# Optimization experiments

Measured on AMD Instinct MI355X. Metric: run time of the kernel, lower is better.

Reference implementation:

```python
import jax, jax.numpy as jnp
import numpy as np

NVOC = 32000
DIM = 512
HID = 512
NLAYERS = 2
SEQ = 128
BATCH = 32


def setup_inputs() -> dict:
    key = jax.random.key(0)
    ks = jax.random.split(key, 8)
    tokens = jax.random.randint(ks[0], (SEQ, BATCH), 0, NVOC, dtype=jnp.int32)
    emb = jax.random.uniform(ks[1], (NVOC, DIM), minval=-0.1, maxval=0.1, dtype=jnp.float32)
    # xavier-uniform-ish init for gate matrices
    def xav(k, shape):
        fan_in, fan_out = shape[1], shape[0]
        lim = jnp.sqrt(6.0 / (fan_in + fan_out))
        return jax.random.uniform(k, shape, minval=-lim, maxval=lim, dtype=jnp.float32)
    W0 = xav(ks[2], (4 * HID, DIM))     # layer 0 input weights
    W1 = xav(ks[3], (4 * HID, HID))     # layer 1 input weights
    U0 = xav(ks[4], (4 * HID, HID))
    U1 = xav(ks[5], (4 * HID, HID))
    b = jnp.zeros((4 * HID,), jnp.float32)
    dec_w = jax.random.uniform(ks[6], (NVOC, HID), minval=-0.1, maxval=0.1, dtype=jnp.float32)
    dec_b = jnp.zeros((NVOC,), jnp.float32)
    return {"tokens": tokens, "emb": emb, "W0": W0, "W1": W1,
            "U0": U0, "U1": U1, "b": b, "dec_w": dec_w, "dec_b": dec_b}


def _lstm_forward(tokens, emb, W0, W1, U0, U1, b, dec_w, dec_b):
    # dropout in eval mode (identity)
    x = emb[tokens]  # [S, B, DIM]
    Ws = [W0, W1]
    Us = [U0, U1]
    h0 = jnp.zeros((NLAYERS, BATCH, HID), x.dtype)
    c0 = jnp.zeros((NLAYERS, BATCH, HID), x.dtype)

    def step(carry, x_t):
        h_tot, c_tot = carry
        new_h, new_c = [], []
        inp = x_t
        for l in range(NLAYERS):
            gates = inp @ Ws[l].T + h_tot[l] @ Us[l].T + b  # [B, 4H]
            i_g, f_g, g_g, o_g = jnp.split(gates, 4, axis=1)
            i_g = jax.nn.sigmoid(i_g)
            f_g = jax.nn.sigmoid(f_g)
            o_g = jax.nn.sigmoid(o_g)
            g_g = jnp.tanh(g_g)
            c_new = f_g * c_tot[l] + i_g * g_g
            h_new = o_g * jnp.tanh(c_new)
            new_h.append(h_new)
            new_c.append(c_new)
            inp = h_new
        return (jnp.stack(new_h), jnp.stack(new_c)), new_h[-1]

    (_, _), outs = jax.lax.scan(step, (h0, c0), x)  # outs: [S, B, HID]
    decoded = outs @ dec_w.T + dec_b  # [S, B, NVOC]
    return decoded


def reference(tokens, emb, W0, W1, U0, U1, b, dec_w, dec_b):
    return _lstm_forward(tokens, emb, W0, W1, U0, U1, b, dec_w, dec_b)
```

## Files before the change

### kernel.cpp

```cpp
#include <hip/hip_runtime.h>
#include <hip/hip_bf16.h>


#define NVOC 32000
#define DIM  512
#define HID  512
#define SEQ  128
#define BAT  32
#define NB   64
#define NDEC 192
#define NTILE (32 * 250)
#define SLOT (BAT * HID)

typedef short s8v __attribute__((ext_vector_type(8)));
typedef short s4v __attribute__((ext_vector_type(4)));
typedef float f4v __attribute__((ext_vector_type(4)));
typedef unsigned long long u64;

__device__ __forceinline__ short f2bf(float f) {
    unsigned u = __builtin_bit_cast(unsigned, f);
    unsigned r = (u + 0x7fffu + ((u >> 16) & 1u)) >> 16;
    return (short)r;
}
__device__ __forceinline__ float bf2f(short s) {
    unsigned u = ((unsigned)(unsigned short)s) << 16;
    return __builtin_bit_cast(float, u);
}
__device__ __forceinline__ float sigm(float x) { return 1.f / (1.f + __expf(-x)); }
__device__ __forceinline__ float ftanh(float x) {
    float e = __expf(2.f * x);
    return 1.f - 2.f / (e + 1.f);
}

__device__ __forceinline__ f4v mf16(s8v a, s8v b, f4v c) {
    return __builtin_amdgcn_mfma_f32_16x16x32_bf16(a, b, c, 0, 0, 0);
}

__device__ __forceinline__ u64 cohload8(const short* p) {
    return __hip_atomic_load((const u64*)p, __ATOMIC_RELAXED,
                             __HIP_MEMORY_SCOPE_AGENT);
}
__device__ __forceinline__ void cohstore2(short* p, unsigned short v) {
    __hip_atomic_store((unsigned short*)p, v, __ATOMIC_RELAXED,
                       __HIP_MEMORY_SCOPE_AGENT);
}

__device__ __forceinline__ bool hasSent(u64 v) {
    u64 n = ~v;
    return ((n - 0x0001000100010001ull) & ~n & 0x8000800080008000ull) != 0ull;
}

__device__ __forceinline__ void poll32s(const unsigned* f, int l, unsigned tgt) {
    const unsigned* p = f + (l & 31);
    while (true) {
        unsigned v = __hip_atomic_load(p, __ATOMIC_RELAXED,
                                       __HIP_MEMORY_SCOPE_AGENT);
        if (__all((int)(v >= tgt))) break;
        __builtin_amdgcn_s_sleep(16);
    }
}

__global__ __launch_bounds__(256) void prep_dec(const float* __restrict__ dw,
                                                short* __restrict__ dbf)
{
    int id = blockIdx.x * 256 + threadIdx.x;
    if (id >= (NVOC * DIM) / 4) return;
    int e = id * 4;
    float4 v = *(const float4*)(dw + e);
    s4v o; o[0] = f2bf(v.x); o[1] = f2bf(v.y); o[2] = f2bf(v.z); o[3] = f2bf(v.w);
    *(s4v*)(dbf + e) = o;
}

__global__ __launch_bounds__(256) void prep_w0(const float* __restrict__ W0,
                                               short* __restrict__ w0h,
                                               short* __restrict__ w0l)
{
    int id = blockIdx.x * 256 + threadIdx.x;
    if (id >= 2048 * 512) return;
    float v = W0[id];
    short h = f2bf(v);
    w0h[id] = h;
    w0l[id] = f2bf(v - bf2f(h));
}

__global__ __launch_bounds__(256) void embed_k(const int* __restrict__ toks,
                                               const float* __restrict__ emb,
                                               short* __restrict__ xemb)
{
    int id = blockIdx.x * 256 + threadIdx.x;
    if (id >= (SEQ * BAT * DIM) / 4) return;
    int e  = id * 4;
    int tb = e >> 9;
    int k4 = e & 511;
    int tok = toks[tb];
    float4 v = *(const float4*)(emb + (size_t)tok * DIM + k4);
    s4v o; o[0] = f2bf(v.x); o[1] = f2bf(v.y); o[2] = f2bf(v.z); o[3] = f2bf(v.w);
    *(s4v*)(xemb + e) = o;
}

__global__ __launch_bounds__(256) void init_k(short* __restrict__ hbuf,
                                              unsigned* __restrict__ bar)
{
    int id = blockIdx.x * 256 + threadIdx.x;
    const int ringU64 = 129 * SLOT / 4;
    if (id < 2 * ringU64) {
        int r = id % ringU64;
        u64 v = (r < SLOT / 4) ? 0ull : 0xFFFFFFFFFFFFFFFFull;
        ((u64*)hbuf)[id] = v;
    }
    if (id < 64) bar[id] = 0;
}

__global__ __launch_bounds__(256) void gx_gemm(
    const short* __restrict__ A,
    const short* __restrict__ Bh,
    const short* __restrict__ Bl,
    float* __restrict__ out)
{
    const int nb = blockIdx.x & 15, mb = blockIdx.x >> 4;
    const int m0 = mb * 128, n0 = nb * 128;
    __shared__ short Alds[128][40];
    __shared__ short Bhl[128][40];
    __shared__ short Bll[128][40];
    const int tid = threadIdx.x, l = tid & 63, w = tid >> 6;
    const int wr = w >> 1, wc = w & 1;
    const int lr = l & 15, kg = l >> 4;

    f4v acc[4][4];
    #pragma unroll
    for (int mi = 0; mi < 4; ++mi)
        #pragma unroll
        for (int ni = 0; ni < 4; ++ni) {
            acc[mi][ni][0] = 0.f; acc[mi][ni][1] = 0.f;
            acc[mi][ni][2] = 0.f; acc[mi][ni][3] = 0.f;
        }

    for (int kt = 0; kt < 16; ++kt) {
        #pragma unroll
        for (int i = 0; i < 2; ++i) {
            int c = tid + i * 256;
            int row = c >> 2, q = (c & 3) << 3;
            *(s8v*)&Alds[row][q] = *(const s8v*)(A  + (size_t)(m0 + row) * 512 + kt * 32 + q);
            *(s8v*)&Bhl[row][q]  = *(const s8v*)(Bh + (size_t)(n0 + row) * 512 + kt * 32 + q);
            *(s8v*)&Bll[row][q]  = *(const s8v*)(Bl + (size_t)(n0 + row) * 512 + kt * 32 + q);
        }
        __syncthreads();
        s8v af[4], bhf[4], blf[4];
        #pragma unroll
        for (int i = 0; i < 4; ++i) {
            af[i]  = *(const s8v*)&Alds[wr * 64 + i * 16 + lr][kg * 8];
            bhf[i] = *(const s8v*)&Bhl[wc * 64 + i * 16 + lr][kg * 8];
            blf[i] = *(const s8v*)&Bll[wc * 64 + i * 16 + lr][kg * 8];
        }
        #pragma unroll
        for (int mi = 0; mi < 4; ++mi)
            #pragma unroll
            for (int ni = 0; ni < 4; ++ni) {
                acc[mi][ni] = mf16(af[mi], bhf[ni], acc[mi][ni]);
                acc[mi][ni] = mf16(af[mi], blf[ni], acc[mi][ni]);
            }
        __syncthreads();
    }

    #pragma unroll
    for (int mi = 0; mi < 4; ++mi)
        #pragma unroll
        for (int ni = 0; ni < 4; ++ni) {
            int n = n0 + wc * 64 + ni * 16 + lr;
            #pragma unroll
            for (int r = 0; r < 4; ++r) {
                int m = m0 + wr * 64 + mi * 16 + kg * 4 + r;
                out[(size_t)m * 2048 + n] = acc[mi][ni][r];
            }
        }
}

__global__ __launch_bounds__(512, 1) void rnn_k(
    const float* __restrict__ W1f, const float* __restrict__ U0f,
    const float* __restrict__ U1f,
    const float* __restrict__ bias,
    const float* __restrict__ Gx,
    short* __restrict__ hbuf,
    short* __restrict__ adec,
    const short* __restrict__ dbf,
    const float* __restrict__ db,
    float* __restrict__ out,
    unsigned* __restrict__ bar)
{
    const int tid = threadIdx.x;
    const int bx  = blockIdx.x;
    const int w2  = tid >> 6;
    const int l   = tid & 63;
    const int lr  = l & 15;
    const int kg  = l >> 4;

    __shared__ short Alds[32][520];
    __shared__ float gbuf[2][4][16][33];
    __shared__ float pbuf[2][4][16][33];
    __shared__ s8v AdT[4][132];
    __shared__ s8v BdT[4][132];

    if (bx >= NB) {
        const int d  = bx - NB;
        const int wm = w2 >> 2;
        const int wn = w2 & 3;
        const int drow = tid >> 2, dq = tid & 3;
        int lastmb = -1;
        for (int tile = d; tile < NTILE; tile += NDEC) {
            const int mb = tile / 250, nbt = tile - mb * 250;
            const int m0 = mb * 128, n0 = nbt * 128;
            if (mb != lastmb) {
                if (w2 == 0) poll32s(bar + 32, l, (unsigned)(4 * mb + 5));
                __syncthreads();
                lastmb = mb;
            }
            f4v acc[4][2];
            #pragma unroll
            for (int mi = 0; mi < 4; ++mi)
                #pragma unroll
                for (int ni = 0; ni < 2; ++ni) {
                    acc[mi][ni][0] = 0.f; acc[mi][ni][1] = 0.f;
                    acc[mi][ni][2] = 0.f; acc[mi][ni][3] = 0.f;
                }
            for (int kt = 0; kt < 16; ++kt) {
                AdT[dq][drow] = *(const s8v*)(adec + (size_t)(m0 + drow) * 512 + kt * 32 + dq * 8);
                BdT[dq][drow] = *(const s8v*)(dbf  + (size_t)(n0 + drow) * 512 + kt * 32 + dq * 8);
                __syncthreads();
                s8v af[4], bfr[2];
                #pragma unroll
                for (int i = 0; i < 4; ++i)
                    af[i] = AdT[kg][wm * 64 + i * 16 + lr];
                #pragma unroll
                for (int j = 0; j < 2; ++j)
                    bfr[j] = BdT[kg][wn * 32 + j * 16 + lr];
                #pragma unroll
                for (int mi = 0; mi < 4; ++mi)
                    #pragma unroll
                    for (int ni = 0; ni < 2; ++ni)
                        acc[mi][ni] = mf16(af[mi], bfr[ni], acc[mi][ni]);
                __syncthreads();
            }
            #pragma unroll
            for (int mi = 0; mi < 4; ++mi)
                #pragma unroll
                for (int ni = 0; ni < 2; ++ni) {
                    int n = n0 + wn * 32 + ni * 16 + lr;
                    float bb = db[n];
                    #pragma unroll
                    for (int r = 0; r < 4; ++r) {
                        int m = m0 + wm * 64 + mi * 16 + kg * 4 + r;
                        out[(size_t)m * NVOC + n] = acc[mi][ni][r] + bb;
                    }
                }
        }
        return;
    }

    const int bl    = bx;
    const int layer = bl >> 5;
    const int j0    = (bl & 31) * 16;
    const int g     = w2 & 3;
    const int kh    = w2 >> 2;

    const int eb = tid >> 4;
    const int ej = tid & 15;
    const int jj = j0 + ej;
    const float bi = bias[jj];
    const float bf_ = bias[512 + jj];
    const float bg = bias[1024 + jj];
    const float bo = bias[1536 + jj];
    float cst = 0.f;

    short* ring0 = hbuf;
    short* ring1 = hbuf + 129 * SLOT;

    auto stageS = [&](const short* s) {
        u64 va[8];
        #pragma unroll
        for (int i = 0; i < 8; ++i) {
            int c = tid + i * 512;
            va[i] = cohload8(s + (c >> 7) * HID + (c & 127) * 4);
        }
        #pragma unroll
        for (int i = 0; i < 8; ++i) {
            int c = tid + i * 512;
            while (hasSent(va[i]))
                va[i] = cohload8(s + (c >> 7) * HID + (c & 127) * 4);
            *(u64*)&Alds[c >> 7][(c & 127) * 4] = va[i];
        }
    };
    auto mfma8 = [&](const s8v* WH, const s8v* WL, float (&dst)[2][4][16][33]) {
        f4v a0h = {0.f, 0.f, 0.f, 0.f};
        f4v a0l = a0h, a1h = a0h, a1l = a0h;
        #pragma unroll
        for (int ks = 0; ks < 8; ++ks) {
            const int k = kh * 256 + ks * 32 + kg * 8;
            s8v a0 = *(const s8v*)&Alds[lr][k];
            s8v a1 = *(const s8v*)&Alds[16 + lr][k];
            a0h = mf16(a0, WH[ks], a0h);
            a0l = mf16(a0, WL[ks], a0l);
            a1h = mf16(a1, WH[ks], a1h);
            a1l = mf16(a1, WL[ks], a1l);
        }
        #pragma unroll
        for (int r = 0; r < 4; ++r) {
            dst[kh][g][lr][kg * 4 + r]      = a0h[r] + a0l[r];
            dst[kh][g][lr][16 + kg * 4 + r] = a1h[r] + a1l[r];
        }
    };
    const int gr = g * 512 + j0 + lr;
    auto loadw = [&](const float* M, s8v* WH, s8v* WL) {
        #pragma unroll
        for (int ks = 0; ks < 8; ++ks) {
            const float* src = M + (size_t)gr * 512 + kh * 256 + ks * 32 + kg * 8;
            float4 va = *(const float4*)src;
            float4 vb = *(const float4*)(src + 4);
            float vv[8] = {va.x, va.y, va.z, va.w, vb.x, vb.y, vb.z, vb.w};
            s8v hi, lo;
            #pragma unroll
            for (int e = 0; e < 8; ++e) {
                short h = f2bf(vv[e]);
                hi[e] = h; lo[e] = f2bf(vv[e] - bf2f(h));
            }
            WH[ks] = hi; WL[ks] = lo;
        }
    };

    if (layer == 0) {
        s8v wh[8], wl[8];
        loadw(U0f, wh, wl);
        for (int it = 0; it < SEQ; ++it) {
            const float* gp = Gx + ((size_t)it * BAT + eb) * 2048 + jj;
            float gx0 = gp[0], gx1 = gp[512], gx2 = gp[1024], gx3 = gp[1536];
            stageS(ring0 + (size_t)it * SLOT);
            __syncthreads();
            mfma8(wh, wl, gbuf);
            __syncthreads();
            float si = gbuf[0][0][ej][eb] + gbuf[1][0][ej][eb] + gx0;
            float sf = gbuf[0][1][ej][eb] + gbuf[1][1][ej][eb] + gx1;
            float sg = gbuf[0][2][ej][eb] + gbuf[1][2][ej][eb] + gx2;
            float so = gbuf[0][3][ej][eb] + gbuf[1][3][ej][eb] + gx3;
            float gi = sigm(si + bi);
            float gf = sigm(sf + bf_);
            float gg = ftanh(sg + bg);
            float go = sigm(so + bo);
            cst = gf * cst + gi * gg;
            unsigned short hs = (unsigned short)f2bf(go * ftanh(cst));
            cohstore2(ring0 + (size_t)(it + 1) * SLOT + eb * HID + jj, hs);
        }
    } else {
        s8v whU[8], wlU[8], whW[8], wlW[8];
        loadw(U1f, whU, wlU);
        loadw(W1f, whW, wlW);
        stageS(ring0 + 1 * SLOT);
        __syncthreads();
        mfma8(whW, wlW, pbuf);
        for (int it = 1; it <= SEQ; ++it) {
            stageS(ring1 + (size_t)(it - 1) * SLOT);
            __syncthreads();
            mfma8(whU, wlU, gbuf);
            __syncthreads();
            float si = gbuf[0][0][ej][eb] + gbuf[1][0][ej][eb]
                     + pbuf[0][0][ej][eb] + pbuf[1][0][ej][eb];
            float sf = gbuf[0][1][ej][eb] + gbuf[1][1][ej][eb]
                     + pbuf[0][1][ej][eb] + pbuf[1][1][ej][eb];
            float sg = gbuf[0][2][ej][eb] + gbuf[1][2][ej][eb]
                     + pbuf[0][2][ej][eb] + pbuf[1][2][ej][eb];
            float so = gbuf[0][3][ej][eb] + gbuf[1][3][ej][eb]
                     + pbuf[0][3][ej][eb] + pbuf[1][3][ej][eb];
            float gi = sigm(si + bi);
            float gf = sigm(sf + bf_);
            float gg = ftanh(sg + bg);
            float go = sigm(so + bo);
            cst = gf * cst + gi * gg;
            unsigned short hs = (unsigned short)f2bf(go * ftanh(cst));
            cohstore2(ring1 + (size_t)it * SLOT + eb * HID + jj, hs);
            cohstore2(adec + ((size_t)(it - 1) * BAT + eb) * HID + jj, hs);
            if ((it & 3) == 0 || it == SEQ) {
                asm volatile("s_waitcnt vmcnt(0)" ::: "memory");
                __syncthreads();
                if (tid == 0)
                    __hip_atomic_store(bar + 32 + (bl & 31), (unsigned)(it + 1),
                                       __ATOMIC_RELAXED, __HIP_MEMORY_SCOPE_AGENT);
            }
            if (it < SEQ) {
                stageS(ring0 + (size_t)(it + 1) * SLOT);
                __syncthreads();
                mfma8(whW, wlW, pbuf);
            }
        }
    }
}

extern "C" void kernel_launch(void* const* d_in, const int* in_sizes, int n_in,
                              void* d_out, int out_size, void* d_ws, size_t ws_size,
                              hipStream_t stream)
{
    const int*   toks = (const int*)d_in[0];
    const float* emb  = (const float*)d_in[1];
    const float* W0   = (const float*)d_in[2];
    const float* W1   = (const float*)d_in[3];
    const float* U0   = (const float*)d_in[4];
    const float* U1   = (const float*)d_in[5];
    const float* bias = (const float*)d_in[6];
    const float* dw   = (const float*)d_in[7];
    const float* db   = (const float*)d_in[8];
    float* out = (float*)d_out;

    char* ws = (char*)d_ws;
    size_t off = 0;
    auto alloc = [&](size_t bytes) -> void* {
        void* p = ws + off;
        off += (bytes + 255) & ~(size_t)255;
        return p;
    };
    short*    dbf  = (short*)alloc((size_t)NVOC * DIM * 2);
    short*    xemb = (short*)alloc((size_t)SEQ * BAT * DIM * 2);
    short*    w0h  = (short*)alloc(2048ull * 512 * 2);
    short*    w0l  = (short*)alloc(2048ull * 512 * 2);
    float*    Gx   = (float*)alloc((size_t)SEQ * BAT * 2048 * 4);
    short*    hbuf = (short*)alloc(2ull * 129 * SLOT * 2);
    short*    adec = (short*)alloc((size_t)SEQ * BAT * HID * 2);
    unsigned* bar  = (unsigned*)alloc(256);

    prep_dec<<<(NVOC * DIM / 4 + 255) / 256, 256, 0, stream>>>(dw, dbf);
    prep_w0 <<<(2048 * 512 + 255) / 256, 256, 0, stream>>>(W0, w0h, w0l);
    embed_k <<<(SEQ * BAT * DIM / 4 + 255) / 256, 256, 0, stream>>>(toks, emb, xemb);
    {
        int ringU64 = 2 * 129 * SLOT / 4;
        init_k<<<(ringU64 + 255) / 256, 256, 0, stream>>>(hbuf, bar);
    }

    gx_gemm<<<32 * 16, 256, 0, stream>>>(xemb, w0h, w0l, Gx);

    rnn_k<<<NB + NDEC, 512, 0, stream>>>(W1, U0, U1, bias, Gx, hbuf, adec,
                                         dbf, db, out, bar);
}
```

Baseline: 699.0 us.

## Merge layer-1 input and recurrent staging into one phase with double-buffered projections

Layer 1 now issues the loads for both its own previous h and layer 0's next h together, stages them side by side in a widened LDS tile, and runs both MFMA passes between a single pair of barriers. The input projection results are double-buffered by parity, so the next step's projection is computed in the same phase as the current recurrence. This removes one stage/sync/MFMA round per timestep from the serial critical path. Row ownership and the per-thread (batch, hidden) mapping are also remapped so each wave owns four units across all four gates, and in layer 0 the Gx loads are placed between issuing and committing the h loads. The cost is more LDS per block and a longer per-step MFMA phase.

```diff
diff --git a/kernel.cpp b/kernel.cpp
--- a/kernel.cpp
+++ b/kernel.cpp
@@ -194,9 +194,9 @@
     const int lr  = l & 15;
     const int kg  = l >> 4;
 
-    __shared__ short Alds[32][520];
-    __shared__ float gbuf[2][4][16][33];
-    __shared__ float pbuf[2][4][16][33];
+    __shared__ short Alds[32][1032];
+    __shared__ float S[2][4][16][33];
+    __shared__ float P[2][2][4][16][33];
     __shared__ s8v AdT[4][132];
     __shared__ s8v BdT[4][132];
 
@@ -259,12 +259,12 @@
     const int bl    = bx;
     const int layer = bl >> 5;
     const int j0    = (bl & 31) * 16;
-    const int g     = w2 & 3;
+    const int wq    = w2 & 3;
     const int kh    = w2 >> 2;
 
-    const int eb = tid >> 4;
-    const int ej = tid & 15;
-    const int jj = j0 + ej;
+    const int jq = l >> 4;
+    const int b  = (l & 15) + kh * 16;
+    const int jj = j0 + wq * 4 + jq;
     const float bi = bias[jj];
     const float bf_ = bias[512 + jj];
     const float bg = bias[1024 + jj];
@@ -274,45 +274,27 @@
     short* ring0 = hbuf;
     short* ring1 = hbuf + 129 * SLOT;
 
-    auto stageS = [&](const short* s) {
-        u64 va[8];
+    auto issue8 = [&](const short* s, u64* va) {
         #pragma unroll
         for (int i = 0; i < 8; ++i) {
             int c = tid + i * 512;
             va[i] = cohload8(s + (c >> 7) * HID + (c & 127) * 4);
         }
+    };
+    auto commit8 = [&](const short* s, u64* va, int c0) {
         #pragma unroll
         for (int i = 0; i < 8; ++i) {
             int c = tid + i * 512;
             while (hasSent(va[i]))
                 va[i] = cohload8(s + (c >> 7) * HID + (c & 127) * 4);
-            *(u64*)&Alds[c >> 7][(c & 127) * 4] = va[i];
+            *(u64*)&Alds[c >> 7][c0 + (c & 127) * 4] = va[i];
         }
     };
-    auto mfma8 = [&](const s8v* WH, const s8v* WL, float (&dst)[2][4][16][33]) {
-        f4v a0h = {0.f, 0.f, 0.f, 0.f};
-        f4v a0l = a0h, a1h = a0h, a1l = a0h;
+    const int grow = (lr >> 2) * 512 + j0 + wq * 4 + (lr & 3);
+    auto loadw = [&](const float* M, s8v* WH, s8v* WL) {
         #pragma unroll
         for (int ks = 0; ks < 8; ++ks) {
-            const int k = kh * 256 + ks * 32 + kg * 8;
-            s8v a0 = *(const s8v*)&Alds[lr][k];
-            s8v a1 = *(const s8v*)&Alds[16 + lr][k];
-            a0h = mf16(a0, WH[ks], a0h);
-            a0l = mf16(a0, WL[ks], a0l);
-            a1h = mf16(a1, WH[ks], a1h);
-            a1l = mf16(a1, WL[ks], a1l);
-        }
-        #pragma unroll
-        for (int r = 0; r < 4; ++r) {
-            dst[kh][g][lr][kg * 4 + r]      = a0h[r] + a0l[r];
-            dst[kh][g][lr][16 + kg * 4 + r] = a1h[r] + a1l[r];
-        }
-    };
-    const int gr = g * 512 + j0 + lr;
-    auto loadw = [&](const float* M, s8v* WH, s8v* WL) {
-        #pragma unroll
-        for (int ks = 0; ks < 8; ++ks) {
-            const float* src = M + (size_t)gr * 512 + kh * 256 + ks * 32 + kg * 8;
+            const float* src = M + (size_t)grow * 512 + kh * 256 + ks * 32 + kg * 8;
             float4 va = *(const float4*)src;
             float4 vb = *(const float4*)(src + 4);
             float vv[8] = {va.x, va.y, va.z, va.w, vb.x, vb.y, vb.z, vb.w};
@@ -325,68 +307,98 @@
             WH[ks] = hi; WL[ks] = lo;
         }
     };
+    auto mfmaS = [&](const s8v* WH, const s8v* WL, int c0,
+                     float (&dst)[2][4][16][33]) {
+        f4v a0h = {0.f, 0.f, 0.f, 0.f};
+        f4v a0l = a0h, a1h = a0h, a1l = a0h;
+        #pragma unroll
+        for (int ks = 0; ks < 8; ++ks) {
+            const int k = c0 + ks * 32 + kg * 8;
+            s8v a0 = *(const s8v*)&Alds[lr][k];
+            s8v a1 = *(const s8v*)&Alds[16 + lr][k];
+            a0h = mf16(a0, WH[ks], a0h);
+            a0l = mf16(a0, WL[ks], a0l);
+            a1h = mf16(a1, WH[ks], a1h);
+            a1l = mf16(a1, WL[ks], a1l);
+        }
+        #pragma unroll
+        for (int r = 0; r < 4; ++r) {
+            dst[kh][wq][lr][kg * 4 + r]      = a0h[r] + a0l[r];
+            dst[kh][wq][lr][16 + kg * 4 + r] = a1h[r] + a1l[r];
+        }
+    };
 
     if (layer == 0) {
         s8v wh[8], wl[8];
         loadw(U0f, wh, wl);
         for (int it = 0; it < SEQ; ++it) {
-            const float* gp = Gx + ((size_t)it * BAT + eb) * 2048 + jj;
+            u64 va[8];
+            issue8(ring0 + (size_t)it * SLOT, va);
+            const float* gp = Gx + ((size_t)it * BAT + b) * 2048 + jj;
             float gx0 = gp[0], gx1 = gp[512], gx2 = gp[1024], gx3 = gp[1536];
-            stageS(ring0 + (size_t)it * SLOT);
-            __syncthreads();
-            mfma8(wh, wl, gbuf);
-            __syncthreads();
-            float si = gbuf[0][0][ej][eb] + gbuf[1][0][ej][eb] + gx0;
-            float sf = gbuf[0][1][ej][eb] + gbuf[1][1][ej][eb] + gx1;
-            float sg = gbuf[0][2][ej][eb] + gbuf[1][2][ej][eb] + gx2;
-            float so = gbuf[0][3][ej][eb] + gbuf[1][3][ej][eb] + gx3;
-            float gi = sigm(si + bi);
-            float gf = sigm(sf + bf_);
-            float gg = ftanh(sg + bg);
-            float go = sigm(so + bo);
+            commit8(ring0 + (size_t)it * SLOT, va, 0);
+            __syncthreads();
+            mfmaS(wh, wl, kh * 256, S);
+            __syncthreads();
+            float gvi = S[0][wq][0 * 4 + jq][b] + S[1][wq][0 * 4 + jq][b] + gx0;
+            float gvf = S[0][wq][1 * 4 + jq][b] + S[1][wq][1 * 4 + jq][b] + gx1;
+            float gvg = S[0][wq][2 * 4 + jq][b] + S[1][wq][2 * 4 + jq][b] + gx2;
+            float gvo = S[0][wq][3 * 4 + jq][b] + S[1][wq][3 * 4 + jq][b] + gx3;
+            float gi = sigm(gvi + bi);
+            float gf = sigm(gvf + bf_);
+            float gg = ftanh(gvg + bg);
+            float go = sigm(gvo + bo);
             cst = gf * cst + gi * gg;
             unsigned short hs = (unsigned short)f2bf(go * ftanh(cst));
-            cohstore2(ring0 + (size_t)(it + 1) * SLOT + eb * HID + jj, hs);
+            cohstore2(ring0 + (size_t)(it + 1) * SLOT + b * HID + jj, hs);
         }
     } else {
         s8v whU[8], wlU[8], whW[8], wlW[8];
         loadw(U1f, whU, wlU);
         loadw(W1f, whW, wlW);
-        stageS(ring0 + 1 * SLOT);
-        __syncthreads();
-        mfma8(whW, wlW, pbuf);
+        {
+            u64 va[8];
+            issue8(ring0 + 1 * SLOT, va);
+            commit8(ring0 + 1 * SLOT, va, 520);
+            __syncthreads();
+            mfmaS(whW, wlW, 520 + kh * 256, P[1]);
+            __syncthreads();
+        }
         for (int it = 1; it <= SEQ; ++it) {
-            stageS(ring1 + (size_t)(it - 1) * SLOT);
-            __syncthreads();
-            mfma8(whU, wlU, gbuf);
-            __syncthreads();
-            float si = gbuf[0][0][ej][eb] + gbuf[1][0][ej][eb]
-                     + pbuf[0][0][ej][eb] + pbuf[1][0][ej][eb];
-            float sf = gbuf[0][1][ej][eb] + gbuf[1][1][ej][eb]
-                     + pbuf[0][1][ej][eb] + pbuf[1][1][ej][eb];
-            float sg = gbuf[0][2][ej][eb] + gbuf[1][2][ej][eb]
-                     + pbuf[0][2][ej][eb] + pbuf[1][2][ej][eb];
-            float so = gbuf[0][3][ej][eb] + gbuf[1][3][ej][eb]
-                     + pbuf[0][3][ej][eb] + pbuf[1][3][ej][eb];
-            float gi = sigm(si + bi);
-            float gf = sigm(sf + bf_);
-            float gg = ftanh(sg + bg);
-            float go = sigm(so + bo);
+            const bool doH0 = (it < SEQ);
+            u64 vh1[8], vh0[8];
+            issue8(ring1 + (size_t)(it - 1) * SLOT, vh1);
+            if (doH0) issue8(ring0 + (size_t)(it + 1) * SLOT, vh0);
+            commit8(ring1 + (size_t)(it - 1) * SLOT, vh1, 0);
+            if (doH0) commit8(ring0 + (size_t)(it + 1) * SLOT, vh0, 520);
+            __syncthreads();
+            mfmaS(whU, wlU, kh * 256, S);
+            if (doH0) mfmaS(whW, wlW, 520 + kh * 256,
+                            P[(it + 1) & 1]);
+            __syncthreads();
+            const int par = it & 1;
+            float gvi = S[0][wq][0 * 4 + jq][b] + S[1][wq][0 * 4 + jq][b]
+                      + P[par][0][wq][0 * 4 + jq][b] + P[par][1][wq][0 * 4 + jq][b];
+            float gvf = S[0][wq][1 * 4 + jq][b] + S[1][wq][1 * 4 + jq][b]
+                      + P[par][0][wq][1 * 4 + jq][b] + P[par][1][wq][1 * 4 + jq][b];
+            float gvg = S[0][wq][2 * 4 + jq][b] + S[1][wq][2 * 4 + jq][b]
+                      + P[par][0][wq][2 * 4 + jq][b] + P[par][1][wq][2 * 4 + jq][b];
+            float gvo = S[0][wq][3 * 4 + jq][b] + S[1][wq][3 * 4 + jq][b]
+                      + P[par][0][wq][3 * 4 + jq][b] + P[par][1][wq][3 * 4 + jq][b];
+            float gi = sigm(gvi + bi);
+            float gf = sigm(gvf + bf_);
+            float gg = ftanh(gvg + bg);
+            float go = sigm(gvo + bo);
             cst = gf * cst + gi * gg;
             unsigned short hs = (unsigned short)f2bf(go * ftanh(cst));
-            cohstore2(ring1 + (size_t)it * SLOT + eb * HID + jj, hs);
-            cohstore2(adec + ((size_t)(it - 1) * BAT + eb) * HID + jj, hs);
+            cohstore2(ring1 + (size_t)it * SLOT + b * HID + jj, hs);
+            cohstore2(adec + ((size_t)(it - 1) * BAT + b) * HID + jj, hs);
             if ((it & 3) == 0 || it == SEQ) {
                 asm volatile("s_waitcnt vmcnt(0)" ::: "memory");
                 __syncthreads();
                 if (tid == 0)
                     __hip_atomic_store(bar + 32 + (bl & 31), (unsigned)(it + 1),
                                        __ATOMIC_RELAXED, __HIP_MEMORY_SCOPE_AGENT);
-            }
-            if (it < SEQ) {
-                stageS(ring0 + (size_t)(it + 1) * SLOT);
-                __syncthreads();
-                mfma8(whW, wlW, pbuf);
             }
         }
     }
```

Result: slower. 1.041 ms (+48.9%).

## Merge prep kernels into one launch and pack LSTM epilogue to two units per thread

Applied to the files above, without the earlier changes.

Combines the four preprocessing kernels (decoder weight cast, W0 hi/lo split, embedding gather, ring init) into a single launch dispatched by block index, removing three kernel launch gaps. In the recurrent kernel, the gate epilogue now runs on half the threads, each handling two adjacent hidden units with float2 Gx loads and one 32-bit packed coherent store instead of two 16-bit stores. Extra __syncthreads are added in layer 1 after the pbuf MFMA so the epilogue threads cannot race with the next pbuf write. This trades fewer, wider stores against idle threads in the epilogue and extra barriers on the serial critical path.

```diff
diff --git a/kernel.cpp b/kernel.cpp
--- a/kernel.cpp
+++ b/kernel.cpp
@@ -40,8 +40,8 @@
     return __hip_atomic_load((const u64*)p, __ATOMIC_RELAXED,
                              __HIP_MEMORY_SCOPE_AGENT);
 }
-__device__ __forceinline__ void cohstore2(short* p, unsigned short v) {
-    __hip_atomic_store((unsigned short*)p, v, __ATOMIC_RELAXED,
+__device__ __forceinline__ void cohstore4(short* p, unsigned v) {
+    __hip_atomic_store((unsigned*)p, v, __ATOMIC_RELAXED,
                        __HIP_MEMORY_SCOPE_AGENT);
 }
 
@@ -60,55 +60,46 @@
     }
 }
 
-__global__ __launch_bounds__(256) void prep_dec(const float* __restrict__ dw,
-                                                short* __restrict__ dbf)
+__global__ __launch_bounds__(256) void prep_all(
+    const float* __restrict__ dw, short* __restrict__ dbf,
+    const float* __restrict__ W0, short* __restrict__ w0h,
+    short* __restrict__ w0l,
+    const int* __restrict__ toks, const float* __restrict__ emb,
+    short* __restrict__ xemb,
+    short* __restrict__ hbuf, unsigned* __restrict__ bar)
 {
-    int id = blockIdx.x * 256 + threadIdx.x;
-    if (id >= (NVOC * DIM) / 4) return;
-    int e = id * 4;
-    float4 v = *(const float4*)(dw + e);
-    s4v o; o[0] = f2bf(v.x); o[1] = f2bf(v.y); o[2] = f2bf(v.z); o[3] = f2bf(v.w);
-    *(s4v*)(dbf + e) = o;
-}
-
-__global__ __launch_bounds__(256) void prep_w0(const float* __restrict__ W0,
-                                               short* __restrict__ w0h,
-                                               short* __restrict__ w0l)
-{
-    int id = blockIdx.x * 256 + threadIdx.x;
-    if (id >= 2048 * 512) return;
-    float v = W0[id];
-    short h = f2bf(v);
-    w0h[id] = h;
-    w0l[id] = f2bf(v - bf2f(h));
-}
-
-__global__ __launch_bounds__(256) void embed_k(const int* __restrict__ toks,
-                                               const float* __restrict__ emb,
-                                               short* __restrict__ xemb)
-{
-    int id = blockIdx.x * 256 + threadIdx.x;
-    if (id >= (SEQ * BAT * DIM) / 4) return;
-    int e  = id * 4;
-    int tb = e >> 9;
-    int k4 = e & 511;
-    int tok = toks[tb];
-    float4 v = *(const float4*)(emb + (size_t)tok * DIM + k4);
-    s4v o; o[0] = f2bf(v.x); o[1] = f2bf(v.y); o[2] = f2bf(v.z); o[3] = f2bf(v.w);
-    *(s4v*)(xemb + e) = o;
-}
-
-__global__ __launch_bounds__(256) void init_k(short* __restrict__ hbuf,
-                                              unsigned* __restrict__ bar)
-{
-    int id = blockIdx.x * 256 + threadIdx.x;
-    const int ringU64 = 129 * SLOT / 4;
-    if (id < 2 * ringU64) {
-        int r = id % ringU64;
-        u64 v = (r < SLOT / 4) ? 0ull : 0xFFFFFFFFFFFFFFFFull;
-        ((u64*)hbuf)[id] = v;
-    }
-    if (id < 64) bar[id] = 0;
+    const int b = blockIdx.x, tid = threadIdx.x;
+    if (b < 16000) {
+        int id = b * 256 + tid;
+        int e = id * 4;
+        float4 v = *(const float4*)(dw + e);
+        s4v o; o[0] = f2bf(v.x); o[1] = f2bf(v.y); o[2] = f2bf(v.z); o[3] = f2bf(v.w);
+        *(s4v*)(dbf + e) = o;
+    } else if (b < 20096) {
+        int id = (b - 16000) * 256 + tid;
+        float v = W0[id];
+        short h = f2bf(v);
+        w0h[id] = h;
+        w0l[id] = f2bf(v - bf2f(h));
+    } else if (b < 22144) {
+        int id = (b - 20096) * 256 + tid;
+        int e  = id * 4;
+        int tb = e >> 9;
+        int k4 = e & 511;
+        int tok = toks[tb];
+        float4 v = *(const float4*)(emb + (size_t)tok * DIM + k4);
+        s4v o; o[0] = f2bf(v.x); o[1] = f2bf(v.y); o[2] = f2bf(v.z); o[3] = f2bf(v.w);
+        *(s4v*)(xemb + e) = o;
+    } else {
+        int id = (b - 22144) * 256 + tid;
+        const int ringU64 = 129 * SLOT / 4;
+        if (id < 2 * ringU64) {
+            int r = id % ringU64;
+            u64 v = (r < SLOT / 4) ? 0ull : 0xFFFFFFFFFFFFFFFFull;
+            ((u64*)hbuf)[id] = v;
+        }
+        if (id < 64) bar[id] = 0;
+    }
 }
 
 __global__ __launch_bounds__(256) void gx_gemm(
@@ -259,17 +250,19 @@
     const int bl    = bx;
     const int layer = bl >> 5;
     const int j0    = (bl & 31) * 16;
-    const int g     = w2 & 3;
-    const int kh    = w2 >> 2;
-
-    const int eb = tid >> 4;
-    const int ej = tid & 15;
-    const int jj = j0 + ej;
-    const float bi = bias[jj];
-    const float bf_ = bias[512 + jj];
-    const float bg = bias[1024 + jj];
-    const float bo = bias[1536 + jj];
-    float cst = 0.f;
+
+    const bool epi = (tid < 256);
+    const int eb  = (tid >> 3) & 31;
+    const int ej  = (tid & 7) * 2;
+    const int jg0 = j0 + ej;
+    float bi0 = 0, bi1 = 0, bff0 = 0, bff1 = 0, bg0 = 0, bg1 = 0, bo0 = 0, bo1 = 0;
+    if (epi) {
+        bi0 = bias[jg0];         bi1 = bias[jg0 + 1];
+        bff0 = bias[512 + jg0];  bff1 = bias[512 + jg0 + 1];
+        bg0 = bias[1024 + jg0];  bg1 = bias[1024 + jg0 + 1];
+        bo0 = bias[1536 + jg0];  bo1 = bias[1536 + jg0 + 1];
+    }
+    float c0 = 0.f, c1 = 0.f;
 
     short* ring0 = hbuf;
     short* ring1 = hbuf + 129 * SLOT;
@@ -289,6 +282,8 @@
             *(u64*)&Alds[c >> 7][(c & 127) * 4] = va[i];
         }
     };
+    const int g  = w2 & 3;
+    const int kh = w2 >> 2;
     auto mfma8 = [&](const s8v* WH, const s8v* WL, float (&dst)[2][4][16][33]) {
         f4v a0h = {0.f, 0.f, 0.f, 0.f};
         f4v a0l = a0h, a1h = a0h, a1l = a0h;
@@ -330,23 +325,37 @@
         s8v wh[8], wl[8];
         loadw(U0f, wh, wl);
         for (int it = 0; it < SEQ; ++it) {
-            const float* gp = Gx + ((size_t)it * BAT + eb) * 2048 + jj;
-            float gx0 = gp[0], gx1 = gp[512], gx2 = gp[1024], gx3 = gp[1536];
+            float2 gxv0 = {0, 0}, gxv1 = {0, 0}, gxv2 = {0, 0}, gxv3 = {0, 0};
+            if (epi) {
+                const float* gp = Gx + ((size_t)it * BAT + eb) * 2048 + jg0;
+                gxv0 = *(const float2*)(gp);
+                gxv1 = *(const float2*)(gp + 512);
+                gxv2 = *(const float2*)(gp + 1024);
+                gxv3 = *(const float2*)(gp + 1536);
+            }
             stageS(ring0 + (size_t)it * SLOT);
             __syncthreads();
             mfma8(wh, wl, gbuf);
             __syncthreads();
-            float si = gbuf[0][0][ej][eb] + gbuf[1][0][ej][eb] + gx0;
-            float sf = gbuf[0][1][ej][eb] + gbuf[1][1][ej][eb] + gx1;
-            float sg = gbuf[0][2][ej][eb] + gbuf[1][2][ej][eb] + gx2;
-            float so = gbuf[0][3][ej][eb] + gbuf[1][3][ej][eb] + gx3;
-            float gi = sigm(si + bi);
-            float gf = sigm(sf + bf_);
-            float gg = ftanh(sg + bg);
-            float go = sigm(so + bo);
-            cst = gf * cst + gi * gg;
-            unsigned short hs = (unsigned short)f2bf(go * ftanh(cst));
-            cohstore2(ring0 + (size_t)(it + 1) * SLOT + eb * HID + jj, hs);
+            if (epi) {
+                float si0 = gbuf[0][0][ej][eb]     + gbuf[1][0][ej][eb]     + gxv0.x;
+                float si1 = gbuf[0][0][ej + 1][eb] + gbuf[1][0][ej + 1][eb] + gxv0.y;
+                float sf0 = gbuf[0][1][ej][eb]     + gbuf[1][1][ej][eb]     + gxv1.x;
+                float sf1 = gbuf[0][1][ej + 1][eb] + gbuf[1][1][ej + 1][eb] + gxv1.y;
+                float sg0 = gbuf[0][2][ej][eb]     + gbuf[1][2][ej][eb]     + gxv2.x;
+                float sg1 = gbuf[0][2][ej + 1][eb] + gbuf[1][2][ej + 1][eb] + gxv2.y;
+                float so0 = gbuf[0][3][ej][eb]     + gbuf[1][3][ej][eb]     + gxv3.x;
+                float so1 = gbuf[0][3][ej + 1][eb] + gbuf[1][3][ej + 1][eb] + gxv3.y;
+                float gi0 = sigm(si0 + bi0), gi1 = sigm(si1 + bi1);
+                float gf0 = sigm(sf0 + bff0), gf1 = sigm(sf1 + bff1);
+                float gg0 = ftanh(sg0 + bg0), gg1 = ftanh(sg1 + bg1);
+                float go0 = sigm(so0 + bo0), go1 = sigm(so1 + bo1);
+                c0 = gf0 * c0 + gi0 * gg0;
+                c1 = gf1 * c1 + gi1 * gg1;
+                unsigned hw = (unsigned)(unsigned short)f2bf(go0 * ftanh(c0)) |
+                              ((unsigned)(unsigned short)f2bf(go1 * ftanh(c1)) << 16);
+                cohstore4(ring0 + (size_t)(it + 1) * SLOT + eb * HID + jg0, hw);
+            }
         }
     } else {
         s8v whU[8], wlU[8], whW[8], wlW[8];
@@ -355,27 +364,41 @@
         stageS(ring0 + 1 * SLOT);
         __syncthreads();
         mfma8(whW, wlW, pbuf);
+        __syncthreads();
         for (int it = 1; it <= SEQ; ++it) {
             stageS(ring1 + (size_t)(it - 1) * SLOT);
             __syncthreads();
             mfma8(whU, wlU, gbuf);
             __syncthreads();
-            float si = gbuf[0][0][ej][eb] + gbuf[1][0][ej][eb]
-                     + pbuf[0][0][ej][eb] + pbuf[1][0][ej][eb];
-            float sf = gbuf[0][1][ej][eb] + gbuf[1][1][ej][eb]
-                     + pbuf[0][1][ej][eb] + pbuf[1][1][ej][eb];
-            float sg = gbuf[0][2][ej][eb] + gbuf[1][2][ej][eb]
-                     + pbuf[0][2][ej][eb] + pbuf[1][2][ej][eb];
-            float so = gbuf[0][3][ej][eb] + gbuf[1][3][ej][eb]
-                     + pbuf[0][3][ej][eb] + pbuf[1][3][ej][eb];
-            float gi = sigm(si + bi);
-            float gf = sigm(sf + bf_);
-            float gg = ftanh(sg + bg);
-            float go = sigm(so + bo);
-            cst = gf * cst + gi * gg;
-            unsigned short hs = (unsigned short)f2bf(go * ftanh(cst));
-            cohstore2(ring1 + (size_t)it * SLOT + eb * HID + jj, hs);
-            cohstore2(adec + ((size_t)(it - 1) * BAT + eb) * HID + jj, hs);
+            unsigned hw = 0;
+            if (epi) {
+                float si0 = gbuf[0][0][ej][eb]     + gbuf[1][0][ej][eb]
+                          + pbuf[0][0][ej][eb]     + pbuf[1][0][ej][eb];
+                float si1 = gbuf[0][0][ej + 1][eb] + gbuf[1][0][ej + 1][eb]
+                          + pbuf[0][0][ej + 1][eb] + pbuf[1][0][ej + 1][eb];
+                float sf0 = gbuf[0][1][ej][eb]     + gbuf[1][1][ej][eb]
+                          + pbuf[0][1][ej][eb]     + pbuf[1][1][ej][eb];
+                float sf1 = gbuf[0][1][ej + 1][eb] + gbuf[1][1][ej + 1][eb]
+                          + pbuf[0][1][ej + 1][eb] + pbuf[1][1][ej + 1][eb];
+                float sg0 = gbuf[0][2][ej][eb]     + gbuf[1][2][ej][eb]
+                          + pbuf[0][2][ej][eb]     + pbuf[1][2][ej][eb];
+                float sg1 = gbuf[0][2][ej + 1][eb] + gbuf[1][2][ej + 1][eb]
+                          + pbuf[0][2][ej + 1][eb] + pbuf[1][2][ej + 1][eb];
+                float so0 = gbuf[0][3][ej][eb]     + gbuf[1][3][ej][eb]
+                          + pbuf[0][3][ej][eb]     + pbuf[1][3][ej][eb];
+                float so1 = gbuf[0][3][ej + 1][eb] + gbuf[1][3][ej + 1][eb]
+                          + pbuf[0][3][ej + 1][eb] + pbuf[1][3][ej + 1][eb];
+                float gi0 = sigm(si0 + bi0), gi1 = sigm(si1 + bi1);
+                float gf0 = sigm(sf0 + bff0), gf1 = sigm(sf1 + bff1);
+                float gg0 = ftanh(sg0 + bg0), gg1 = ftanh(sg1 + bg1);
+                float go0 = sigm(so0 + bo0), go1 = sigm(so1 + bo1);
+                c0 = gf0 * c0 + gi0 * gg0;
+                c1 = gf1 * c1 + gi1 * gg1;
+                hw = (unsigned)(unsigned short)f2bf(go0 * ftanh(c0)) |
+                     ((unsigned)(unsigned short)f2bf(go1 * ftanh(c1)) << 16);
+                cohstore4(ring1 + (size_t)it * SLOT + eb * HID + jg0, hw);
+                cohstore4(adec + ((size_t)(it - 1) * BAT + eb) * HID + jg0, hw);
+            }
             if ((it & 3) == 0 || it == SEQ) {
                 asm volatile("s_waitcnt vmcnt(0)" ::: "memory");
                 __syncthreads();
@@ -387,6 +410,7 @@
                 stageS(ring0 + (size_t)(it + 1) * SLOT);
                 __syncthreads();
                 mfma8(whW, wlW, pbuf);
+                __syncthreads();
             }
         }
     }
@@ -423,13 +447,8 @@
     short*    adec = (short*)alloc((size_t)SEQ * BAT * HID * 2);
     unsigned* bar  = (unsigned*)alloc(256);
 
-    prep_dec<<<(NVOC * DIM / 4 + 255) / 256, 256, 0, stream>>>(dw, dbf);
-    prep_w0 <<<(2048 * 512 + 255) / 256, 256, 0, stream>>>(W0, w0h, w0l);
-    embed_k <<<(SEQ * BAT * DIM / 4 + 255) / 256, 256, 0, stream>>>(toks, emb, xemb);
-    {
-        int ringU64 = 2 * 129 * SLOT / 4;
-        init_k<<<(ringU64 + 255) / 256, 256, 0, stream>>>(hbuf, bar);
-    }
+    prep_all<<<26272, 256, 0, stream>>>(dw, dbf, W0, w0h, w0l,
+                                        toks, emb, xemb, hbuf, bar);
 
     gx_gemm<<<32 * 16, 256, 0, stream>>>(xemb, w0h, w0l, Gx);
 
```

Result: no change. 695.5 us, median of 3 (-0.5%).
